# Kernel optimization log

Hardware: AMD Instinct MI355X
Metric: run time of the kernel (lower is better)

Reference implementation:

```python
import jax, jax.numpy as jnp
import numpy as np
from jax import lax

# Sign table S[m, j, k]: output blade m = sum_{j,k} S[m,j,k] * conv_j(a_k),
# transcribed directly from apply_ga3. Blade order: 0,1,2,3,12,23,13,123.
_TERMS = [
    [(0,0,1),(1,1,1),(2,2,1),(3,3,1),(4,4,-1),(5,5,-1),(6,6,-1),(7,7,-1)],
    [(1,0,1),(0,1,1),(2,4,1),(4,2,-1),(3,6,1),(6,3,-1),(5,7,-1),(7,5,-1)],
    [(2,0,1),(0,2,1),(1,4,-1),(4,1,1),(3,5,1),(5,3,-1),(6,7,1),(7,6,1)],
    [(3,0,1),(0,3,1),(1,6,-1),(6,1,1),(2,5,-1),(5,2,1),(4,7,-1),(7,4,-1)],
    [(4,0,1),(0,4,1),(2,1,1),(1,2,-1),(3,7,1),(7,3,1),(6,5,1),(5,6,-1)],
    [(5,0,1),(0,5,1),(3,2,1),(2,3,-1),(1,7,1),(7,1,1),(4,6,1),(6,4,-1)],
    [(6,0,1),(0,6,1),(3,1,1),(1,3,-1),(2,7,-1),(7,2,-1),(5,4,1),(4,5,-1)],
    [(7,0,1),(0,7,1),(5,1,1),(1,5,1),(6,2,-1),(2,6,-1),(4,3,1),(3,4,1)],
]
_S = np.zeros((8, 8, 8), dtype=np.float32)
for m, terms in enumerate(_TERMS):
    for j, k, s in terms:
        _S[m, j, k] = s
SIGNS = jnp.asarray(_S)


def setup_inputs() -> dict:
    key = jax.random.key(0)
    k1, k2, k3 = jax.random.split(key, 3)
    B, Cin, Cout, H = 8, 16, 16, 128
    x = jax.random.normal(k1, (B, 8 * Cin, H, H), dtype=jnp.float32)
    # Kaiming-uniform-ish small init like nn.Conv2d default scale
    fan_in = Cin * 9
    bound = 1.0 / np.sqrt(fan_in)
    W = jax.random.uniform(k2, (8, Cout, Cin, 3, 3), dtype=jnp.float32,
                           minval=-bound, maxval=bound)
    b = jax.random.uniform(k3, (8, Cout), dtype=jnp.float32,
                           minval=-bound, maxval=bound)
    return {"x": x, "W": W, "b": b}


def reference(x, W, b):
    # x: [B, 8*Cin, H, W] (channel c -> blade c%8, group c//8)
    # W: [8, Cout, Cin, kh, kw]; b: [8, Cout]
    B, C, H, Wd = x.shape
    nW, Cout, Cin, kh, kw = W.shape
    # Split interleaved blades: a[k] = x[:, k::8]  -> [8, B, Cin, H, W]
    a = x.reshape(B, Cin, 8, H, Wd).transpose(2, 0, 1, 3, 4)
    a = a.reshape(8 * B, Cin, H, Wd)                     # fold blade k into batch
    W_all = W.reshape(8 * Cout, Cin, kh, kw)             # all 8 convs at once
    pad = [(1, 1), (1, 1)]
    f = lax.conv_general_dilated(a, W_all, window_strides=(1, 1), padding=pad)
    f = f + b.reshape(1, 8 * Cout, 1, 1)
    Ho, Wo = f.shape[-2:]
    f = f.reshape(8, B, 8, Cout, Ho, Wo)                 # [k, B, j, Cout, H', W']
    # out[m] = sum_{j,k} S[m,j,k] * conv_j(a_k)
    out = jnp.einsum('mjk,kbjchw->bcmhw', SIGNS, f)
    # make_ga3: interleave blades back into channels
    return out.reshape(B, Cout * 8, Ho, Wo)
```

## Files before the change

### kernel.cpp

```cpp
#include <hip/hip_runtime.h>
#include <stdint.h>
#include <stddef.h>


typedef __attribute__((ext_vector_type(8))) short short8;
typedef __attribute__((ext_vector_type(4))) float f32x4;

__device__ __constant__ int c_J[64] = {
  0,1,2,3,4,5,6,7,
  1,0,4,6,2,7,3,5,
  2,4,0,5,1,3,7,6,
  3,6,5,0,7,2,1,4,
  4,2,1,7,0,6,5,3,
  5,7,3,2,6,0,4,1,
  6,3,7,1,5,4,0,2,
  7,5,6,4,3,1,2,0
};
__device__ __constant__ float c_Sg[64] = {
  1,1,1,1,-1,-1,-1,-1,
  1,1,-1,-1,1,-1,1,-1,
  1,1,1,-1,-1,1,1,1,
  1,1,1,1,-1,-1,-1,-1,
  1,1,-1,1,1,1,-1,1,
  1,1,1,-1,-1,1,1,1,
  1,1,-1,-1,1,-1,1,-1,
  1,1,-1,1,1,1,-1,1
};

__device__ inline unsigned short f2bf(float f) {
  unsigned int u = __float_as_uint(f);
  u += 0x7FFFu + ((u >> 16) & 1u);
  return (unsigned short)(u >> 16);
}

__global__ __launch_bounds__(256) void border_kernel(unsigned short* __restrict__ xt) {
  const int b = blockIdx.y;
  const int g = blockIdx.x * 256 + threadIdx.x;
  const int p = g >> 6, u = g & 63;
  int h, w;
  if (p < 130)      { h = 0;       w = p; }
  else if (p < 260) { h = 129;     w = p - 130; }
  else if (p < 388) { h = p - 259; w = 0; }
  else              { h = p - 387; w = 129; }
  *(unsigned int*)(xt + ((size_t)(b * 130 + h) * 130 + w) * 128 + 2 * u) = 0u;
}

__global__ __launch_bounds__(256) void xpose_kernel(const float* __restrict__ x,
                                                    unsigned short* __restrict__ xt) {
  __shared__ unsigned short t[128 * 33];
  const int wt  = blockIdx.x;
  const int h   = blockIdx.y;
  const int b   = blockIdx.z;
  const int tid = threadIdx.x;
  const int w0  = wt * 32;
  const int wl  = tid & 31;
  const int ic0 = tid >> 5;
  #pragma unroll
  for (int i = 0; i < 16; ++i) {
    int ic = ic0 + i * 8;
    float v = x[((size_t)(b * 128 + ic) * 128 + h) * 128 + w0 + wl];
    t[ic * 33 + wl] = f2bf(v);
  }
  __syncthreads();
  #pragma unroll
  for (int i = 0; i < 8; ++i) {
    int q = tid + i * 256;
    int w = q >> 6;
    int p = q & 63;
    unsigned int lo = t[(2 * p) * 33 + w];
    unsigned int hi = t[(2 * p + 1) * 33 + w];
    size_t off = ((size_t)(b * 130 + h + 1) * 130 + (w0 + w + 1)) * 128 + 2 * p;
    *(unsigned int*)(xt + off) = lo | (hi << 16);
  }
}

__global__ __launch_bounds__(256) void wprep_kernel(const float* __restrict__ W,
                                                    const float* __restrict__ bias,
                                                    unsigned short* __restrict__ vt,
                                                    float* __restrict__ beff) {
  int gid = blockIdx.x * 256 + threadIdx.x;
  int t   = gid >> 14;
  int rem = gid & 16383;
  int oc  = rem >> 7;
  int ic  = rem & 127;
  int m = oc & 7, cout = oc >> 3;
  int k = ic & 7, cin = ic >> 3;
  int j = c_J[m * 8 + k];
  float s = c_Sg[m * 8 + k];
  float val = s * W[((j * 16 + cout) * 16 + cin) * 9 + t];
  int ks = ic >> 5, quad = (ic >> 3) & 3, e = ic & 7;
  int ocb = oc >> 4, l15 = oc & 15;
  vt[(size_t)((t * 4 + ks) * 8 + ocb) * 512 + (quad * 16 + l15) * 8 + e] = f2bf(val);
  if (gid < 128) {
    int m2 = gid & 7, cout2 = gid >> 3;
    float acc = 0.f;
    #pragma unroll
    for (int kk = 0; kk < 8; ++kk)
      acc += c_Sg[m2 * 8 + kk] * bias[c_J[m2 * 8 + kk] * 16 + cout2];
    beff[gid] = acc;
  }
}

__global__ __launch_bounds__(256) void conv_kernel(const unsigned short* __restrict__ xt,
                                                   const unsigned short* __restrict__ vt,
                                                   const float* __restrict__ beff,
                                                   float* __restrict__ out) {
  __shared__ __align__(16) unsigned short lds_x[10 * 18 * 128];
  const int tid  = threadIdx.x;
  const int bx   = blockIdx.x;
  const int by   = blockIdx.y;
  const int b    = blockIdx.z;
  const int lane = tid & 63;
  const int wave = tid >> 6;
  const int wm   = wave >> 1;
  const int wn   = wave & 1;
  const int l15  = lane & 15;
  const int quad = lane >> 4;

  {
    const unsigned short* xb = xt + ((size_t)(b * 130 + by * 8) * 130 + bx * 16) * 128;
    #pragma unroll
    for (int i = 0; i < 11; ++i) {
      int c  = tid + i * 256;
      int hh = c / 288;
      int r  = c - hh * 288;
      uint4 v = *((const uint4*)(xb + (size_t)hh * (130 * 128)) + r);
      ((uint4*)lds_x)[c ^ ((c >> 4) & 7)] = v;
    }
    if (tid < 64) {
      int c  = tid + 2816;
      int hh = c / 288;
      int r  = c - hh * 288;
      uint4 v = *((const uint4*)(xb + (size_t)hh * (130 * 128)) + r);
      ((uint4*)lds_x)[c ^ ((c >> 4) & 7)] = v;
    }
  }
  __syncthreads();

  f32x4 acc[4][4];
  #pragma unroll
  for (int mi = 0; mi < 4; ++mi)
    #pragma unroll
    for (int ni = 0; ni < 4; ++ni)
      acc[mi][ni] = f32x4{0.f, 0.f, 0.f, 0.f};

  const unsigned short* vtw = vt + (size_t)(wn * 4) * 512 + (size_t)lane * 8;

  #pragma unroll
  for (int t = 0; t < 9; ++t) {
    const int dh = t / 3, dw = t % 3;
    int rowb[4];
    #pragma unroll
    for (int mi = 0; mi < 4; ++mi)
      rowb[mi] = (wm * 4 + mi + dh) * 18 + l15 + dw;
    #pragma unroll
    for (int ks = 0; ks < 4; ++ks) {
      short8 bb[4];
      #pragma unroll
      for (int ni = 0; ni < 4; ++ni)
        bb[ni] = *(const short8*)(vtw + (size_t)((t * 4 + ks) * 8 + ni) * 512);
      short8 a[4];
      #pragma unroll
      for (int mi = 0; mi < 4; ++mi) {
        int row = rowb[mi];
        int off = row * 256 + ((ks * 64 + quad * 16) ^ ((row & 7) << 4));
        a[mi] = *(const short8*)((const char*)lds_x + off);
      }
      #pragma unroll
      for (int mi = 0; mi < 4; ++mi)
        #pragma unroll
        for (int ni = 0; ni < 4; ++ni)
          acc[mi][ni] = __builtin_amdgcn_mfma_f32_16x16x32_bf16(a[mi], bb[ni], acc[mi][ni], 0, 0, 0);
    }
  }

  const int h0 = by * 8, w0 = bx * 16;
  #pragma unroll
  for (int ni = 0; ni < 4; ++ni) {
    int oc = (wn * 4 + ni) * 16 + l15;
    float bv = beff[oc];
    #pragma unroll
    for (int mi = 0; mi < 4; ++mi) {
      int h = h0 + wm * 4 + mi;
      int w = w0 + quad * 4;
      f32x4 v = acc[mi][ni];
      v[0] += bv; v[1] += bv; v[2] += bv; v[3] += bv;
      *(f32x4*)(out + ((size_t)(b * 128 + oc) * 128 + h) * 128 + w) = v;
    }
  }
}

extern "C" void kernel_launch(void* const* d_in, const int* in_sizes, int n_in,
                              void* d_out, int out_size, void* d_ws, size_t ws_size,
                              hipStream_t stream) {
  (void)in_sizes; (void)n_in; (void)out_size; (void)ws_size;
  const float* x    = (const float*)d_in[0];
  const float* W    = (const float*)d_in[1];
  const float* bias = (const float*)d_in[2];
  float* out = (float*)d_out;

  const size_t XT_BYTES = (size_t)8 * 130 * 130 * 128 * 2;
  const size_t VT_BYTES = (size_t)9 * 4 * 8 * 512 * 2;
  unsigned short* xt = (unsigned short*)d_ws;
  unsigned short* vt = (unsigned short*)((char*)d_ws + XT_BYTES);
  float* beff = (float*)((char*)d_ws + XT_BYTES + VT_BYTES);

  border_kernel<<<dim3(129, 8), 256, 0, stream>>>(xt);
  xpose_kernel<<<dim3(4, 128, 8), 256, 0, stream>>>(x, xt);
  wprep_kernel<<<dim3(576), 256, 0, stream>>>(W, bias, vt, beff);
  conv_kernel<<<dim3(8, 16, 8), 256, 0, stream>>>(xt, vt, beff, out);
}
```

Baseline: 158.0 us.

## Merge border and weight prep kernels; process two row tiles per conv block with prefetch

The border-zeroing and weight-prep kernels are merged into one launch, which saves a kernel launch. The conv kernel now handles two row tiles per block (rows by0*8 and by0*8+64), so the grid is halved. The second tile's input halo is loaded into registers while the first tile computes, which hides global load latency. The cost is higher register pressure (12 uint4 held plus the accumulators) and half as many blocks, which may reduce occupancy on the 256 CUs.

```diff
diff --git a/kernel.cpp b/kernel.cpp
--- a/kernel.cpp
+++ b/kernel.cpp
@@ -33,18 +33,6 @@
   return (unsigned short)(u >> 16);
 }
 
-__global__ __launch_bounds__(256) void border_kernel(unsigned short* __restrict__ xt) {
-  const int b = blockIdx.y;
-  const int g = blockIdx.x * 256 + threadIdx.x;
-  const int p = g >> 6, u = g & 63;
-  int h, w;
-  if (p < 130)      { h = 0;       w = p; }
-  else if (p < 260) { h = 129;     w = p - 130; }
-  else if (p < 388) { h = p - 259; w = 0; }
-  else              { h = p - 387; w = 129; }
-  *(unsigned int*)(xt + ((size_t)(b * 130 + h) * 130 + w) * 128 + 2 * u) = 0u;
-}
-
 __global__ __launch_bounds__(256) void xpose_kernel(const float* __restrict__ x,
                                                     unsigned short* __restrict__ xt) {
   __shared__ unsigned short t[128 * 33];
@@ -74,30 +62,45 @@
   }
 }
 
-__global__ __launch_bounds__(256) void wprep_kernel(const float* __restrict__ W,
-                                                    const float* __restrict__ bias,
-                                                    unsigned short* __restrict__ vt,
-                                                    float* __restrict__ beff) {
-  int gid = blockIdx.x * 256 + threadIdx.x;
-  int t   = gid >> 14;
-  int rem = gid & 16383;
-  int oc  = rem >> 7;
-  int ic  = rem & 127;
-  int m = oc & 7, cout = oc >> 3;
-  int k = ic & 7, cin = ic >> 3;
-  int j = c_J[m * 8 + k];
-  float s = c_Sg[m * 8 + k];
-  float val = s * W[((j * 16 + cout) * 16 + cin) * 9 + t];
-  int ks = ic >> 5, quad = (ic >> 3) & 3, e = ic & 7;
-  int ocb = oc >> 4, l15 = oc & 15;
-  vt[(size_t)((t * 4 + ks) * 8 + ocb) * 512 + (quad * 16 + l15) * 8 + e] = f2bf(val);
-  if (gid < 128) {
-    int m2 = gid & 7, cout2 = gid >> 3;
-    float acc = 0.f;
-    #pragma unroll
-    for (int kk = 0; kk < 8; ++kk)
-      acc += c_Sg[m2 * 8 + kk] * bias[c_J[m2 * 8 + kk] * 16 + cout2];
-    beff[gid] = acc;
+__global__ __launch_bounds__(256) void prep_kernel(const float* __restrict__ W,
+                                                   const float* __restrict__ bias,
+                                                   unsigned short* __restrict__ vt,
+                                                   float* __restrict__ beff,
+                                                   unsigned short* __restrict__ xt) {
+  const int bid = blockIdx.x;
+  if (bid < 576) {
+    int gid = bid * 256 + threadIdx.x;
+    int t   = gid >> 14;
+    int rem = gid & 16383;
+    int oc  = rem >> 7;
+    int ic  = rem & 127;
+    int m = oc & 7, cout = oc >> 3;
+    int k = ic & 7, cin = ic >> 3;
+    int j = c_J[m * 8 + k];
+    float s = c_Sg[m * 8 + k];
+    float val = s * W[((j * 16 + cout) * 16 + cin) * 9 + t];
+    int ks = ic >> 5, quad = (ic >> 3) & 3, e = ic & 7;
+    int ocb = oc >> 4, l15 = oc & 15;
+    vt[(size_t)((t * 4 + ks) * 8 + ocb) * 512 + (quad * 16 + l15) * 8 + e] = f2bf(val);
+    if (gid < 128) {
+      int m2 = gid & 7, cout2 = gid >> 3;
+      float acc = 0.f;
+      #pragma unroll
+      for (int kk = 0; kk < 8; ++kk)
+        acc += c_Sg[m2 * 8 + kk] * bias[c_J[m2 * 8 + kk] * 16 + cout2];
+      beff[gid] = acc;
+    }
+  } else {
+    int g2 = (bid - 576) * 256 + threadIdx.x;
+    int b  = g2 / 33024;
+    int g  = g2 - b * 33024;
+    const int p = g >> 6, u = g & 63;
+    int h, w;
+    if (p < 130)      { h = 0;       w = p; }
+    else if (p < 260) { h = 129;     w = p - 130; }
+    else if (p < 388) { h = p - 259; w = 0; }
+    else              { h = p - 387; w = 129; }
+    *(unsigned int*)(xt + ((size_t)(b * 130 + h) * 130 + w) * 128 + 2 * u) = 0u;
   }
 }
 
@@ -108,7 +111,7 @@
   __shared__ __align__(16) unsigned short lds_x[10 * 18 * 128];
   const int tid  = threadIdx.x;
   const int bx   = blockIdx.x;
-  const int by   = blockIdx.y;
+  const int by0  = blockIdx.y;
   const int b    = blockIdx.z;
   const int lane = tid & 63;
   const int wave = tid >> 6;
@@ -117,75 +120,100 @@
   const int l15  = lane & 15;
   const int quad = lane >> 4;
 
-  {
-    const unsigned short* xb = xt + ((size_t)(b * 130 + by * 8) * 130 + bx * 16) * 128;
-    #pragma unroll
-    for (int i = 0; i < 11; ++i) {
-      int c  = tid + i * 256;
+  const unsigned short* xb0 = xt + ((size_t)(b * 130 + by0 * 8) * 130 + bx * 16) * 128;
+  const unsigned short* xb1 = xb0 + (size_t)64 * 130 * 128;
+
+  uint4 pre[12];
+  #pragma unroll
+  for (int i = 0; i < 12; ++i) {
+    int c = tid + i * 256;
+    if (i < 11 || tid < 64) {
       int hh = c / 288;
       int r  = c - hh * 288;
-      uint4 v = *((const uint4*)(xb + (size_t)hh * (130 * 128)) + r);
-      ((uint4*)lds_x)[c ^ ((c >> 4) & 7)] = v;
-    }
-    if (tid < 64) {
-      int c  = tid + 2816;
+      pre[i] = *((const uint4*)(xb0 + (size_t)hh * (130 * 128)) + r);
+    }
+  }
+  #pragma unroll
+  for (int i = 0; i < 12; ++i) {
+    int c = tid + i * 256;
+    if (i < 11 || tid < 64)
+      ((uint4*)lds_x)[c ^ ((c >> 4) & 7)] = pre[i];
+  }
+  __syncthreads();
+
+  #pragma unroll
+  for (int i = 0; i < 12; ++i) {
+    int c = tid + i * 256;
+    if (i < 11 || tid < 64) {
       int hh = c / 288;
       int r  = c - hh * 288;
-      uint4 v = *((const uint4*)(xb + (size_t)hh * (130 * 128)) + r);
-      ((uint4*)lds_x)[c ^ ((c >> 4) & 7)] = v;
-    }
-  }
-  __syncthreads();
-
-  f32x4 acc[4][4];
-  #pragma unroll
-  for (int mi = 0; mi < 4; ++mi)
-    #pragma unroll
-    for (int ni = 0; ni < 4; ++ni)
-      acc[mi][ni] = f32x4{0.f, 0.f, 0.f, 0.f};
+      pre[i] = *((const uint4*)(xb1 + (size_t)hh * (130 * 128)) + r);
+    }
+  }
 
   const unsigned short* vtw = vt + (size_t)(wn * 4) * 512 + (size_t)lane * 8;
 
   #pragma unroll
-  for (int t = 0; t < 9; ++t) {
-    const int dh = t / 3, dw = t % 3;
-    int rowb[4];
+  for (int tile = 0; tile < 2; ++tile) {
+    f32x4 acc[4][4];
     #pragma unroll
     for (int mi = 0; mi < 4; ++mi)
-      rowb[mi] = (wm * 4 + mi + dh) * 18 + l15 + dw;
+      #pragma unroll
+      for (int ni = 0; ni < 4; ++ni)
+        acc[mi][ni] = f32x4{0.f, 0.f, 0.f, 0.f};
+
     #pragma unroll
-    for (int ks = 0; ks < 4; ++ks) {
-      short8 bb[4];
-      #pragma unroll
-      for (int ni = 0; ni < 4; ++ni)
-        bb[ni] = *(const short8*)(vtw + (size_t)((t * 4 + ks) * 8 + ni) * 512);
-      short8 a[4];
-      #pragma unroll
-      for (int mi = 0; mi < 4; ++mi) {
-        int row = rowb[mi];
-        int off = row * 256 + ((ks * 64 + quad * 16) ^ ((row & 7) << 4));
-        a[mi] = *(const short8*)((const char*)lds_x + off);
-      }
+    for (int t = 0; t < 9; ++t) {
+      const int dh = t / 3, dw = t % 3;
+      int rowb[4];
       #pragma unroll
       for (int mi = 0; mi < 4; ++mi)
+        rowb[mi] = (wm * 4 + mi + dh) * 18 + l15 + dw;
+      #pragma unroll
+      for (int ks = 0; ks < 4; ++ks) {
+        short8 bb[4];
         #pragma unroll
         for (int ni = 0; ni < 4; ++ni)
-          acc[mi][ni] = __builtin_amdgcn_mfma_f32_16x16x32_bf16(a[mi], bb[ni], acc[mi][ni], 0, 0, 0);
-    }
-  }
-
-  const int h0 = by * 8, w0 = bx * 16;
-  #pragma unroll
-  for (int ni = 0; ni < 4; ++ni) {
-    int oc = (wn * 4 + ni) * 16 + l15;
-    float bv = beff[oc];
+          bb[ni] = *(const short8*)(vtw + (size_t)((t * 4 + ks) * 8 + ni) * 512);
+        short8 a[4];
+        #pragma unroll
+        for (int mi = 0; mi < 4; ++mi) {
+          int row = rowb[mi];
+          int off = row * 256 + ((ks * 64 + quad * 16) ^ ((row & 7) << 4));
+          a[mi] = *(const short8*)((const char*)lds_x + off);
+        }
+        #pragma unroll
+        for (int mi = 0; mi < 4; ++mi)
+          #pragma unroll
+          for (int ni = 0; ni < 4; ++ni)
+            acc[mi][ni] = __builtin_amdgcn_mfma_f32_16x16x32_bf16(a[mi], bb[ni], acc[mi][ni], 0, 0, 0);
+      }
+    }
+
+    const int h0 = by0 * 8 + tile * 64, w0 = bx * 16;
     #pragma unroll
-    for (int mi = 0; mi < 4; ++mi) {
-      int h = h0 + wm * 4 + mi;
-      int w = w0 + quad * 4;
-      f32x4 v = acc[mi][ni];
-      v[0] += bv; v[1] += bv; v[2] += bv; v[3] += bv;
-      *(f32x4*)(out + ((size_t)(b * 128 + oc) * 128 + h) * 128 + w) = v;
+    for (int ni = 0; ni < 4; ++ni) {
+      int oc = (wn * 4 + ni) * 16 + l15;
+      float bv = beff[oc];
+      #pragma unroll
+      for (int mi = 0; mi < 4; ++mi) {
+        int h = h0 + wm * 4 + mi;
+        int w = w0 + quad * 4;
+        f32x4 v = acc[mi][ni];
+        v[0] += bv; v[1] += bv; v[2] += bv; v[3] += bv;
+        *(f32x4*)(out + ((size_t)(b * 128 + oc) * 128 + h) * 128 + w) = v;
+      }
+    }
+
+    if (tile == 0) {
+      __syncthreads();
+      #pragma unroll
+      for (int i = 0; i < 12; ++i) {
+        int c = tid + i * 256;
+        if (i < 11 || tid < 64)
+          ((uint4*)lds_x)[c ^ ((c >> 4) & 7)] = pre[i];
+      }
+      __syncthreads();
     }
   }
 }
@@ -205,8 +233,7 @@
   unsigned short* vt = (unsigned short*)((char*)d_ws + XT_BYTES);
   float* beff = (float*)((char*)d_ws + XT_BYTES + VT_BYTES);
 
-  border_kernel<<<dim3(129, 8), 256, 0, stream>>>(xt);
+  prep_kernel<<<dim3(1608), 256, 0, stream>>>(W, bias, vt, beff, xt);
   xpose_kernel<<<dim3(4, 128, 8), 256, 0, stream>>>(x, xt);
-  wprep_kernel<<<dim3(576), 256, 0, stream>>>(W, bias, vt, beff);
-  conv_kernel<<<dim3(8, 16, 8), 256, 0, stream>>>(xt, vt, beff, out);
-}
+  conv_kernel<<<dim3(8, 8, 8), 256, 0, stream>>>(xt, vt, beff, out);
+}
```

New measurement: 192.1 us. 21.5% more time.

## Merge border and weight prep kernels; retile conv waves to 2x8 MFMA blocks

Applied to the files above, without the earlier changes.

Merges the border-zeroing and weight-prep kernels into one launch, removing one kernel launch. The conv kernel changes its wave tiling from a 2x2 wave grid (4 rows x 4 oc-blocks each) to 4 waves each covering 2 rows x all 8 oc-blocks. Each wave now reads fewer A fragments from LDS but twice as many B fragments from global/L2. The change also adds s_setprio around the MFMA bursts and a launch bound of 3 blocks per CU to control occupancy.

```diff
diff --git a/kernel.cpp b/kernel.cpp
--- a/kernel.cpp
+++ b/kernel.cpp
@@ -33,18 +33,6 @@
   return (unsigned short)(u >> 16);
 }
 
-__global__ __launch_bounds__(256) void border_kernel(unsigned short* __restrict__ xt) {
-  const int b = blockIdx.y;
-  const int g = blockIdx.x * 256 + threadIdx.x;
-  const int p = g >> 6, u = g & 63;
-  int h, w;
-  if (p < 130)      { h = 0;       w = p; }
-  else if (p < 260) { h = 129;     w = p - 130; }
-  else if (p < 388) { h = p - 259; w = 0; }
-  else              { h = p - 387; w = 129; }
-  *(unsigned int*)(xt + ((size_t)(b * 130 + h) * 130 + w) * 128 + 2 * u) = 0u;
-}
-
 __global__ __launch_bounds__(256) void xpose_kernel(const float* __restrict__ x,
                                                     unsigned short* __restrict__ xt) {
   __shared__ unsigned short t[128 * 33];
@@ -74,37 +62,52 @@
   }
 }
 
-__global__ __launch_bounds__(256) void wprep_kernel(const float* __restrict__ W,
-                                                    const float* __restrict__ bias,
-                                                    unsigned short* __restrict__ vt,
-                                                    float* __restrict__ beff) {
-  int gid = blockIdx.x * 256 + threadIdx.x;
-  int t   = gid >> 14;
-  int rem = gid & 16383;
-  int oc  = rem >> 7;
-  int ic  = rem & 127;
-  int m = oc & 7, cout = oc >> 3;
-  int k = ic & 7, cin = ic >> 3;
-  int j = c_J[m * 8 + k];
-  float s = c_Sg[m * 8 + k];
-  float val = s * W[((j * 16 + cout) * 16 + cin) * 9 + t];
-  int ks = ic >> 5, quad = (ic >> 3) & 3, e = ic & 7;
-  int ocb = oc >> 4, l15 = oc & 15;
-  vt[(size_t)((t * 4 + ks) * 8 + ocb) * 512 + (quad * 16 + l15) * 8 + e] = f2bf(val);
-  if (gid < 128) {
-    int m2 = gid & 7, cout2 = gid >> 3;
-    float acc = 0.f;
-    #pragma unroll
-    for (int kk = 0; kk < 8; ++kk)
-      acc += c_Sg[m2 * 8 + kk] * bias[c_J[m2 * 8 + kk] * 16 + cout2];
-    beff[gid] = acc;
-  }
-}
-
-__global__ __launch_bounds__(256) void conv_kernel(const unsigned short* __restrict__ xt,
-                                                   const unsigned short* __restrict__ vt,
-                                                   const float* __restrict__ beff,
-                                                   float* __restrict__ out) {
+__global__ __launch_bounds__(256) void prep_kernel(const float* __restrict__ W,
+                                                   const float* __restrict__ bias,
+                                                   unsigned short* __restrict__ vt,
+                                                   float* __restrict__ beff,
+                                                   unsigned short* __restrict__ xt) {
+  const int bid = blockIdx.x;
+  if (bid < 576) {
+    int gid = bid * 256 + threadIdx.x;
+    int t   = gid >> 14;
+    int rem = gid & 16383;
+    int oc  = rem >> 7;
+    int ic  = rem & 127;
+    int m = oc & 7, cout = oc >> 3;
+    int k = ic & 7, cin = ic >> 3;
+    int j = c_J[m * 8 + k];
+    float s = c_Sg[m * 8 + k];
+    float val = s * W[((j * 16 + cout) * 16 + cin) * 9 + t];
+    int ks = ic >> 5, quad = (ic >> 3) & 3, e = ic & 7;
+    int ocb = oc >> 4, l15 = oc & 15;
+    vt[(size_t)((t * 4 + ks) * 8 + ocb) * 512 + (quad * 16 + l15) * 8 + e] = f2bf(val);
+    if (gid < 128) {
+      int m2 = gid & 7, cout2 = gid >> 3;
+      float acc = 0.f;
+      #pragma unroll
+      for (int kk = 0; kk < 8; ++kk)
+        acc += c_Sg[m2 * 8 + kk] * bias[c_J[m2 * 8 + kk] * 16 + cout2];
+      beff[gid] = acc;
+    }
+  } else {
+    int g2 = (bid - 576) * 256 + threadIdx.x;
+    int b  = g2 / 33024;
+    int g  = g2 - b * 33024;
+    const int p = g >> 6, u = g & 63;
+    int h, w;
+    if (p < 130)      { h = 0;       w = p; }
+    else if (p < 260) { h = 129;     w = p - 130; }
+    else if (p < 388) { h = p - 259; w = 0; }
+    else              { h = p - 387; w = 129; }
+    *(unsigned int*)(xt + ((size_t)(b * 130 + h) * 130 + w) * 128 + 2 * u) = 0u;
+  }
+}
+
+__global__ __launch_bounds__(256, 3) void conv_kernel(const unsigned short* __restrict__ xt,
+                                                      const unsigned short* __restrict__ vt,
+                                                      const float* __restrict__ beff,
+                                                      float* __restrict__ out) {
   __shared__ __align__(16) unsigned short lds_x[10 * 18 * 128];
   const int tid  = threadIdx.x;
   const int bx   = blockIdx.x;
@@ -112,8 +115,6 @@
   const int b    = blockIdx.z;
   const int lane = tid & 63;
   const int wave = tid >> 6;
-  const int wm   = wave >> 1;
-  const int wn   = wave & 1;
   const int l15  = lane & 15;
   const int quad = lane >> 4;
 
@@ -137,51 +138,53 @@
   }
   __syncthreads();
 
-  f32x4 acc[4][4];
-  #pragma unroll
-  for (int mi = 0; mi < 4; ++mi)
-    #pragma unroll
-    for (int ni = 0; ni < 4; ++ni)
+  f32x4 acc[2][8];
+  #pragma unroll
+  for (int mi = 0; mi < 2; ++mi)
+    #pragma unroll
+    for (int ni = 0; ni < 8; ++ni)
       acc[mi][ni] = f32x4{0.f, 0.f, 0.f, 0.f};
 
-  const unsigned short* vtw = vt + (size_t)(wn * 4) * 512 + (size_t)lane * 8;
+  const unsigned short* vtw = vt + (size_t)lane * 8;
 
   #pragma unroll
   for (int t = 0; t < 9; ++t) {
     const int dh = t / 3, dw = t % 3;
-    int rowb[4];
-    #pragma unroll
-    for (int mi = 0; mi < 4; ++mi)
-      rowb[mi] = (wm * 4 + mi + dh) * 18 + l15 + dw;
+    int rowb[2];
+    #pragma unroll
+    for (int mi = 0; mi < 2; ++mi)
+      rowb[mi] = (wave * 2 + mi + dh) * 18 + l15 + dw;
     #pragma unroll
     for (int ks = 0; ks < 4; ++ks) {
-      short8 bb[4];
-      #pragma unroll
-      for (int ni = 0; ni < 4; ++ni)
+      short8 bb[8];
+      #pragma unroll
+      for (int ni = 0; ni < 8; ++ni)
         bb[ni] = *(const short8*)(vtw + (size_t)((t * 4 + ks) * 8 + ni) * 512);
-      short8 a[4];
-      #pragma unroll
-      for (int mi = 0; mi < 4; ++mi) {
+      short8 a[2];
+      #pragma unroll
+      for (int mi = 0; mi < 2; ++mi) {
         int row = rowb[mi];
         int off = row * 256 + ((ks * 64 + quad * 16) ^ ((row & 7) << 4));
         a[mi] = *(const short8*)((const char*)lds_x + off);
       }
-      #pragma unroll
-      for (int mi = 0; mi < 4; ++mi)
+      __builtin_amdgcn_s_setprio(1);
+      #pragma unroll
+      for (int mi = 0; mi < 2; ++mi)
         #pragma unroll
-        for (int ni = 0; ni < 4; ++ni)
+        for (int ni = 0; ni < 8; ++ni)
           acc[mi][ni] = __builtin_amdgcn_mfma_f32_16x16x32_bf16(a[mi], bb[ni], acc[mi][ni], 0, 0, 0);
+      __builtin_amdgcn_s_setprio(0);
     }
   }
 
   const int h0 = by * 8, w0 = bx * 16;
   #pragma unroll
-  for (int ni = 0; ni < 4; ++ni) {
-    int oc = (wn * 4 + ni) * 16 + l15;
+  for (int ni = 0; ni < 8; ++ni) {
+    int oc = ni * 16 + l15;
     float bv = beff[oc];
     #pragma unroll
-    for (int mi = 0; mi < 4; ++mi) {
-      int h = h0 + wm * 4 + mi;
+    for (int mi = 0; mi < 2; ++mi) {
+      int h = h0 + wave * 2 + mi;
       int w = w0 + quad * 4;
       f32x4 v = acc[mi][ni];
       v[0] += bv; v[1] += bv; v[2] += bv; v[3] += bv;
@@ -205,8 +208,7 @@
   unsigned short* vt = (unsigned short*)((char*)d_ws + XT_BYTES);
   float* beff = (float*)((char*)d_ws + XT_BYTES + VT_BYTES);
 
-  border_kernel<<<dim3(129, 8), 256, 0, stream>>>(xt);
+  prep_kernel<<<dim3(1608), 256, 0, stream>>>(W, bias, vt, beff, xt);
   xpose_kernel<<<dim3(4, 128, 8), 256, 0, stream>>>(x, xt);
-  wprep_kernel<<<dim3(576), 256, 0, stream>>>(W, bias, vt, beff);
   conv_kernel<<<dim3(8, 16, 8), 256, 0, stream>>>(xt, vt, beff, out);
 }
```

Result: slower. 170.9 us (+8.1%).
